# Optimization experiments

Measured on AMD Instinct MI355X. Metric: run time of the kernel, lower is better.

Reference implementation:

```python
import jax, jax.numpy as jnp
import numpy as np
import math

B, S, E, HEAD = 4, 2048, 1024, 64  # num_heads=16 -> head_size = 1024//16


def setup_inputs() -> dict:
    key = jax.random.key(0)
    kx, kp, kq, kk, kv = jax.random.split(key, 5)
    std = math.sqrt(2.0 / (E + HEAD))
    return {
        "x": jax.random.normal(kx, (B, S, E), dtype=jnp.float32),
        "padding_mask": jax.random.randint(kp, (B, S), 0, 2, dtype=jnp.int32),
        "Wq": jax.random.normal(kq, (HEAD, E), dtype=jnp.float32) * std,
        "Wk": jax.random.normal(kk, (HEAD, E), dtype=jnp.float32) * std,
        "Wv": jax.random.normal(kv, (HEAD, E), dtype=jnp.float32) * std,
    }


def reference(x, padding_mask, Wq, Wk, Wv):
    # q,k,v: [B,S,head] via Linear (x @ W.T, no bias)
    q = jnp.einsum("bse,he->bsh", x, Wq)
    k = jnp.einsum("bse,he->bsh", x, Wk)
    v = jnp.einsum("bse,he->bsh", x, Wv)
    scores = jnp.einsum("bqh,bkh->bqk", q, k)  # [B,S,S]
    seq = x.shape[1]
    causal = jnp.tril(jnp.ones((seq, seq), dtype=jnp.float32))  # [S,S]
    mask = causal[None, :, :] * padding_mask.astype(jnp.float32)[:, None, :]  # [B,S,S]
    scores = jnp.where(mask == 0, jnp.float32(-1e9), scores)
    head_size = k.shape[-1]
    attn = jax.nn.softmax(scores / jnp.sqrt(jnp.float32(head_size)), axis=-1)
    return jnp.einsum("bqk,bkh->bqh", attn, v)
```

## Files before the change

### kernel.cpp

```cpp
#include <hip/hip_runtime.h>
#include <hip/hip_bf16.h>
#include <math.h>

#define B_ 4
#define S_ 2048
#define E_ 1024
#define H_ 64
#define NQT 32
#define SPLITS 8
#define TPS 4

typedef short bf16x8 __attribute__((ext_vector_type(8)));
typedef float f32x4 __attribute__((ext_vector_type(4)));
typedef unsigned short u16x8 __attribute__((ext_vector_type(8)));
typedef unsigned short u16x4 __attribute__((ext_vector_type(4)));

__device__ __forceinline__ unsigned short f2bf(float f){
    unsigned u = __builtin_bit_cast(unsigned, f);
    u += 0x7fffu + ((u >> 16) & 1u);
    return (unsigned short)(u >> 16);
}
__device__ __forceinline__ float bf2f(unsigned short h){
    return __builtin_bit_cast(float, ((unsigned)h) << 16);
}
#define MFMA16(a,b,c) __builtin_amdgcn_mfma_f32_16x16x32_bf16((a),(b),(c),0,0,0)

__device__ __forceinline__ void gload_lds16(const void* g, void* l){
    __builtin_amdgcn_global_load_lds((const __attribute__((address_space(1))) unsigned int*)g,
                                     (__attribute__((address_space(3))) unsigned int*)l, 16, 0, 0);
}

__global__ __launch_bounds__(256) void wprep_kernel(
    const float* __restrict__ Wq, const float* __restrict__ Wk,
    const float* __restrict__ Wv,
    unsigned short* __restrict__ WhiS, unsigned short* __restrict__ WloS)
{
    const int gid = blockIdx.x*256 + threadIdx.x;
    const int n = gid >> 7, g = gid & 127;
    const float* W = (n < 64)  ? (Wq + (size_t)n*E_)
                   : (n < 128) ? (Wk + (size_t)(n-64)*E_)
                               : (Wv + (size_t)(n-128)*E_);
    const int gs = (g & ~7) | ((g & 7) ^ (n & 7));
    const float* src = W + gs*8;
    float4 a = ((const float4*)src)[0];
    float4 b = ((const float4*)src)[1];
    float vv[8] = {a.x,a.y,a.z,a.w,b.x,b.y,b.z,b.w};
    u16x8 hv, lv;
    #pragma unroll
    for (int j=0;j<8;j++){ unsigned short h = f2bf(vv[j]); hv[j]=h; lv[j]=f2bf(vv[j]-bf2f(h)); }
    ((u16x8*)WhiS)[n*128 + g] = hv;
    ((u16x8*)WloS)[n*128 + g] = lv;
}

__global__ __launch_bounds__(256) void qkv_kernel(
    const float* __restrict__ x,
    const unsigned short* __restrict__ WhiS, const unsigned short* __restrict__ WloS,
    unsigned short* __restrict__ Qhi, unsigned short* __restrict__ Qlo,
    unsigned short* __restrict__ Khi, unsigned short* __restrict__ Klo,
    unsigned short* __restrict__ Vt)
{
    __shared__ unsigned short Ah[32*64], Al[32*64];
    __shared__ unsigned short Bh[192*64], Bl[192*64];
    const int m0 = blockIdx.x * 32;
    const int tid = threadIdx.x;
    const int lane = tid & 63, wv = tid >> 6, l15 = lane & 15, quad = lane >> 4;

    f32x4 acc[2][3];
    #pragma unroll
    for (int mt=0;mt<2;mt++)
    #pragma unroll
    for (int nt=0;nt<3;nt++) acc[mt][nt] = f32x4{0.f,0.f,0.f,0.f};

    const int arow = tid >> 3;
    const int ag   = tid & 7;
    unsigned short* tbuf = (wv < 2) ? Bh : Bl;
    const unsigned short* gsrc = (wv < 2) ? WhiS : WloS;
    const int rbase0 = (wv & 1) * 96;
    const int lrow = lane >> 3, lgrp = lane & 7;

    for (int k0 = 0; k0 < E_; k0 += 64) {
        const float* xs = x + (size_t)(m0 + arow)*E_ + k0 + ag*8;
        float4 xa = ((const float4*)xs)[0];
        float4 xb = ((const float4*)xs)[1];
        __syncthreads();
        #pragma unroll
        for (int i = 0; i < 12; i++) {
            const int rb = rbase0 + i*8;
            const unsigned short* gp = gsrc + (size_t)(rb + lrow)*E_ + k0 + lgrp*8;
            gload_lds16(gp, tbuf + rb*64);
        }
        {
            float vv[8] = {xa.x,xa.y,xa.z,xa.w,xb.x,xb.y,xb.z,xb.w};
            u16x8 hv, lv;
            #pragma unroll
            for (int j=0;j<8;j++){ unsigned short h = f2bf(vv[j]); hv[j]=h; lv[j]=f2bf(vv[j]-bf2f(h)); }
            const int idx = arow*8 + (ag ^ (arow & 7));
            ((u16x8*)Ah)[idx] = hv; ((u16x8*)Al)[idx] = lv;
        }
        __syncthreads();
        #pragma unroll
        for (int kk=0; kk<2; kk++){
            const int xr = (kk*4+quad) ^ (l15 & 7);
            bf16x8 ah[2], al[2];
            #pragma unroll
            for (int mt=0; mt<2; mt++){
                const int arw = mt*16 + l15;
                ah[mt] = ((const bf16x8*)Ah)[arw*8 + xr];
                al[mt] = ((const bf16x8*)Al)[arw*8 + xr];
            }
            #pragma unroll
            for (int nt=0; nt<3; nt++){
                const int brw = wv*48 + nt*16 + l15;
                bf16x8 bh = ((const bf16x8*)Bh)[brw*8 + xr];
                bf16x8 bl = ((const bf16x8*)Bl)[brw*8 + xr];
                #pragma unroll
                for (int mt=0; mt<2; mt++){
                    acc[mt][nt] = MFMA16(ah[mt], bh, acc[mt][nt]);
                    acc[mt][nt] = MFMA16(ah[mt], bl, acc[mt][nt]);
                    acc[mt][nt] = MFMA16(al[mt], bh, acc[mt][nt]);
                }
            }
        }
    }
    #pragma unroll
    for (int nt=0; nt<3; nt++){
        const int n = wv*48 + nt*16 + l15;
        const int comp = n >> 6, c = n & 63;
        if (comp < 2) {
            unsigned short* dh = (comp==0) ? Qhi : Khi;
            unsigned short* dl = (comp==0) ? Qlo : Klo;
            #pragma unroll
            for (int mt=0; mt<2; mt++)
            #pragma unroll
            for (int r=0; r<4; r++){
                const int row = m0 + mt*16 + quad*4 + r;
                float v = acc[mt][nt][r];
                unsigned short h = f2bf(v);
                dh[(size_t)row*H_ + c] = h;
                dl[(size_t)row*H_ + c] = f2bf(v - bf2f(h));
            }
        } else {
            #pragma unroll
            for (int mt=0; mt<2; mt++){
                const int m = m0 + mt*16 + quad*4;
                const int b = m >> 11, s0 = m & (S_-1);
                u16x4 pk;
                #pragma unroll
                for (int r=0;r<4;r++) pk[r] = f2bf(acc[mt][nt][r]);
                *(u16x4*)(Vt + (size_t)(b*H_ + c)*S_ + s0) = pk;
            }
        }
    }
}

__global__ __launch_bounds__(256) void meanv_kernel(const unsigned short* __restrict__ Vt,
                                                    float* __restrict__ meanV)
{
    int b = blockIdx.x >> 6, h = blockIdx.x & 63;
    const unsigned short* src = Vt + (size_t)b*H_*S_ + (size_t)h*S_;
    float sum = 0.f;
    for (int j = threadIdx.x; j < S_; j += 256) sum += bf2f(src[j]);
    #pragma unroll
    for (int m=32; m>=1; m>>=1) sum += __shfl_xor(sum, m);
    __shared__ float red[4];
    if ((threadIdx.x & 63) == 0) red[threadIdx.x >> 6] = sum;
    __syncthreads();
    if (threadIdx.x == 0) meanV[b*H_ + h] = (red[0]+red[1]+red[2]+red[3]) * (1.f/S_);
}

__global__ __launch_bounds__(256) void attn_kernel(
    const unsigned short* __restrict__ Qhi, const unsigned short* __restrict__ Qlo,
    const unsigned short* __restrict__ Khi, const unsigned short* __restrict__ Klo,
    const unsigned short* __restrict__ Vt, const int* __restrict__ pad,
    float* __restrict__ Opart, float* __restrict__ mpart, float* __restrict__ lpart)
{
    const int qt = blockIdx.x, b = blockIdx.y, sp = blockIdx.z;
    const int t0 = sp * TPS;
    if (t0 > qt) return;
    const int t1 = min(t0 + TPS, qt + 1);

    __shared__ unsigned short Ps[4][64*20];

    const int tid = threadIdx.x, lane = tid & 63, wv = tid >> 6, l15 = lane & 15, quad = lane >> 4;

    const size_t qrow = (size_t)(b*S_ + qt*64 + wv*16 + l15);
    bf16x8 aqh0 = *(const bf16x8*)(Qhi + qrow*H_ + quad*8);
    bf16x8 aqh1 = *(const bf16x8*)(Qhi + qrow*H_ + 32 + quad*8);
    bf16x8 aql0 = *(const bf16x8*)(Qlo + qrow*H_ + quad*8);
    bf16x8 aql1 = *(const bf16x8*)(Qlo + qrow*H_ + 32 + quad*8);

    const unsigned short* KhB = Khi + (size_t)(b*S_)*H_;
    const unsigned short* KlB = Klo + (size_t)(b*S_)*H_;
    const unsigned short* VB  = Vt  + (size_t)b*H_*S_;
    const int* padB = pad + b*S_;

    float m_i[4], l_i[4];
    f32x4 o[4];
    #pragma unroll
    for (int r=0;r<4;r++){ m_i[r] = -INFINITY; l_i[r] = 0.f; }
    #pragma unroll
    for (int i=0;i<4;i++) o[i] = f32x4{0.f,0.f,0.f,0.f};

    const int qg = qt*64 + wv*16 + quad*4;
    unsigned short* Pw = &Ps[wv][0];

    for (int t = t0; t < t1; ++t) {
        const int kb = t * 64;

        int pv[4];
        #pragma unroll
        for (int nt=0; nt<4; nt++) pv[nt] = padB[kb + nt*16 + l15];

        f32x4 s[4];
        #pragma unroll
        for (int nt=0; nt<4; nt++){
            const size_t krow = (size_t)(kb + nt*16 + l15)*H_;
            bf16x8 bh0 = *(const bf16x8*)(KhB + krow + quad*8);
            bf16x8 bh1 = *(const bf16x8*)(KhB + krow + 32 + quad*8);
            bf16x8 bl0 = *(const bf16x8*)(KlB + krow + quad*8);
            bf16x8 bl1 = *(const bf16x8*)(KlB + krow + 32 + quad*8);
            f32x4 z = f32x4{0.f,0.f,0.f,0.f};
            z = MFMA16(aqh0, bh0, z);
            z = MFMA16(aqh1, bh1, z);
            z = MFMA16(aqh0, bl0, z);
            z = MFMA16(aqh1, bl1, z);
            z = MFMA16(aql0, bh0, z);
            z = MFMA16(aql1, bh1, z);
            s[nt] = z;
        }
        float rmax[4] = {-INFINITY,-INFINITY,-INFINITY,-INFINITY};
        #pragma unroll
        for (int nt=0; nt<4; nt++){
            const int kg = kb + nt*16 + l15;
            #pragma unroll
            for (int r=0;r<4;r++){
                bool ok = (kg <= qg + r) && (pv[nt] != 0);
                float v = ok ? s[nt][r]*0.125f : -1.25e8f;
                s[nt][r] = v;
                rmax[r] = fmaxf(rmax[r], v);
            }
        }
        #pragma unroll
        for (int msk=1; msk<=8; msk<<=1){
            #pragma unroll
            for (int r=0;r<4;r++) rmax[r] = fmaxf(rmax[r], __shfl_xor(rmax[r], msk));
        }
        float alpha[4];
        #pragma unroll
        for (int r=0;r<4;r++){
            float mn = fmaxf(m_i[r], rmax[r]);
            alpha[r] = __expf(m_i[r] - mn);
            m_i[r] = mn;
        }
        float rsum[4] = {0.f,0.f,0.f,0.f};
        #pragma unroll
        for (int nt=0; nt<4; nt++)
        #pragma unroll
        for (int r=0;r<4;r++){
            float p = __expf(s[nt][r] - m_i[r]);
            s[nt][r] = p;
            rsum[r] += p;
        }
        #pragma unroll
        for (int msk=1; msk<=8; msk<<=1){
            #pragma unroll
            for (int r=0;r<4;r++) rsum[r] += __shfl_xor(rsum[r], msk);
        }
        #pragma unroll
        for (int r=0;r<4;r++) l_i[r] = l_i[r]*alpha[r] + rsum[r];
        #pragma unroll
        for (int hnt=0; hnt<4; hnt++)
        #pragma unroll
        for (int r=0;r<4;r++) o[hnt][r] *= alpha[r];

        #pragma unroll
        for (int nt=0; nt<4; nt++){
            const int key = nt*16 + l15;
            u16x4 pk;
            #pragma unroll
            for (int r=0;r<4;r++) pk[r] = f2bf(s[nt][r]);
            *(u16x4*)(Pw + key*20 + quad*4) = pk;
        }
        #pragma unroll
        for (int ks=0; ks<2; ks++){
            bf16x8 ap;
            #pragma unroll
            for (int j=0;j<8;j++) ap[j] = (short)Pw[(ks*32 + quad*8 + j)*20 + l15];
            #pragma unroll
            for (int hnt=0; hnt<4; hnt++){
                bf16x8 bv = *(const bf16x8*)(VB + (size_t)(hnt*16 + l15)*S_ + kb + ks*32 + quad*8);
                o[hnt] = MFMA16(ap, bv, o[hnt]);
            }
        }
    }
    const size_t rbase = ((size_t)((b*NQT + qt)*SPLITS + sp))*64 + wv*16 + quad*4;
    if (l15 == 0) {
        #pragma unroll
        for (int r=0;r<4;r++){ mpart[rbase + r] = m_i[r]; lpart[rbase + r] = l_i[r]; }
    }
    #pragma unroll
    for (int hnt=0; hnt<4; hnt++)
    #pragma unroll
    for (int r=0;r<4;r++)
        Opart[(rbase + r)*H_ + hnt*16 + l15] = o[hnt][r];
}

__global__ __launch_bounds__(256) void combine_kernel(
    const float* __restrict__ Opart, const float* __restrict__ mpart,
    const float* __restrict__ lpart, const float* __restrict__ meanV,
    float* __restrict__ out)
{
    const int idx = blockIdx.x*256 + threadIdx.x;
    const int h = idx & 63;
    const int q = (idx >> 6) & (S_-1);
    const int b = idx >> 17;
    const int qt = q >> 6, r = q & 63;
    const int ns = (qt >> 2) + 1;
    const size_t rb = ((size_t)(b*NQT + qt)*SPLITS)*64 + r;
    float M = -INFINITY;
    for (int s2=0; s2<ns; s2++) M = fmaxf(M, mpart[rb + (size_t)s2*64]);
    float res;
    if (M == -1.25e8f) {
        res = meanV[b*H_ + h];
    } else {
        float L = 0.f, acc = 0.f;
        for (int s2=0; s2<ns; s2++){
            float mi = mpart[rb + (size_t)s2*64];
            float wgt = __expf(mi - M);
            L += wgt * lpart[rb + (size_t)s2*64];
            acc += wgt * Opart[(rb + (size_t)s2*64)*H_ + h];
        }
        res = acc / L;
    }
    out[idx] = res;
}

extern "C" void kernel_launch(void* const* d_in, const int* in_sizes, int n_in,
                              void* d_out, int out_size, void* d_ws, size_t ws_size,
                              hipStream_t stream)
{
    (void)in_sizes; (void)n_in; (void)out_size; (void)ws_size;
    const float* x  = (const float*)d_in[0];
    const int* pad  = (const int*)d_in[1];
    const float* Wq = (const float*)d_in[2];
    const float* Wk = (const float*)d_in[3];
    const float* Wv = (const float*)d_in[4];
    float* out = (float*)d_out;
    char* ws = (char*)d_ws;
    const size_t MB = 1u << 20;
    unsigned short* Qhi = (unsigned short*)(ws + 0*MB);
    unsigned short* Qlo = (unsigned short*)(ws + 1*MB);
    unsigned short* Khi = (unsigned short*)(ws + 2*MB);
    unsigned short* Klo = (unsigned short*)(ws + 3*MB);
    unsigned short* Vt  = (unsigned short*)(ws + 4*MB);
    float* Opart = (float*)(ws + 5*MB);
    float* mpart = (float*)(ws + 21*MB);
    float* lpart = (float*)(ws + 21*MB + (1u<<18));
    float* meanV = (float*)(ws + 21*MB + 2*(1u<<18));
    unsigned short* WhiS = (unsigned short*)(ws + 22*MB);
    unsigned short* WloS = (unsigned short*)(ws + 22*MB + 512*1024);

    wprep_kernel<<<dim3(96), 256, 0, stream>>>(Wq, Wk, Wv, WhiS, WloS);
    qkv_kernel<<<dim3(256), 256, 0, stream>>>(x, WhiS, WloS, Qhi, Qlo, Khi, Klo, Vt);
    meanv_kernel<<<dim3(256), 256, 0, stream>>>(Vt, meanV);
    attn_kernel<<<dim3(NQT, B_, SPLITS), 256, 0, stream>>>(Qhi, Qlo, Khi, Klo, Vt, pad,
                                                           Opart, mpart, lpart);
    combine_kernel<<<dim3((B_*S_*H_)/256), 256, 0, stream>>>(Opart, mpart, lpart, meanV, out);
}
```

Before: 162.2 us.

## Stage K/V tiles through double-buffered swizzled LDS with register prefetch

Each block now loads its K-hi, K-lo, V and padding tiles cooperatively into double-buffered shared memory. Three wavefronts each fetch one tensor and the fourth fetches the mask, and the next tile is prefetched into registers during compute. The previous code had every wavefront read all four K/V tiles straight from global memory, so the same data was fetched four times per block. The XOR swizzle is meant to avoid LDS bank conflicts, and the causal comparison is skipped on off-diagonal tiles. In exchange it uses about 50KB of LDS, which may lower occupancy, and adds a block barrier per tile.

Measured after the change: 142.3 us. 12.3% less time.

```diff
diff --git a/kernel.cpp b/kernel.cpp
--- a/kernel.cpp
+++ b/kernel.cpp
@@ -179,9 +179,12 @@
     if (t0 > qt) return;
     const int t1 = min(t0 + TPS, qt + 1);
 
+    __shared__ unsigned short KtH[2][64*64], KtL[2][64*64], Vts[2][64*64];
     __shared__ unsigned short Ps[4][64*20];
+    __shared__ int pad_s[2][64];
 
     const int tid = threadIdx.x, lane = tid & 63, wv = tid >> 6, l15 = lane & 15, quad = lane >> 4;
+    const int role = tid >> 6, srow = tid & 63;
 
     const size_t qrow = (size_t)(b*S_ + qt*64 + wv*16 + l15);
     bf16x8 aqh0 = *(const bf16x8*)(Qhi + qrow*H_ + quad*8);
@@ -204,21 +207,52 @@
     const int qg = qt*64 + wv*16 + quad*4;
     unsigned short* Pw = &Ps[wv][0];
 
+    u16x8 stg[8];
+    int pvreg = 0;
+    auto issue = [&](int t){
+        const int kb = t * 64;
+        if (role < 3) {
+            const unsigned short* gs =
+                (role==0) ? (KhB + (size_t)(kb + srow)*H_) :
+                (role==1) ? (KlB + (size_t)(kb + srow)*H_) :
+                            (VB + (size_t)srow*S_ + kb);
+            #pragma unroll
+            for (int i=0;i<8;i++) stg[i] = ((const u16x8*)gs)[i];
+        } else {
+            pvreg = padB[kb + srow];
+        }
+    };
+    auto commit = [&](int buf){
+        if (role < 3) {
+            unsigned short* ld = (role==0) ? &KtH[buf][0] : (role==1) ? &KtL[buf][0] : &Vts[buf][0];
+            #pragma unroll
+            for (int i=0;i<8;i++) ((u16x8*)ld)[srow*8 + (i ^ (srow & 7))] = stg[i];
+        } else {
+            pad_s[buf][srow] = pvreg;
+        }
+    };
+
+    issue(t0); commit(0);
+    __syncthreads();
+    int cur = 0;
+
     for (int t = t0; t < t1; ++t) {
         const int kb = t * 64;
+        const bool hasnext = (t + 1 < t1);
+        if (hasnext) issue(t + 1);
 
         int pv[4];
         #pragma unroll
-        for (int nt=0; nt<4; nt++) pv[nt] = padB[kb + nt*16 + l15];
+        for (int nt=0; nt<4; nt++) pv[nt] = pad_s[cur][nt*16 + l15];
 
         f32x4 s[4];
         #pragma unroll
         for (int nt=0; nt<4; nt++){
-            const size_t krow = (size_t)(kb + nt*16 + l15)*H_;
-            bf16x8 bh0 = *(const bf16x8*)(KhB + krow + quad*8);
-            bf16x8 bh1 = *(const bf16x8*)(KhB + krow + 32 + quad*8);
-            bf16x8 bl0 = *(const bf16x8*)(KlB + krow + quad*8);
-            bf16x8 bl1 = *(const bf16x8*)(KlB + krow + 32 + quad*8);
+            const int krw = nt*16 + l15;
+            bf16x8 bh0 = ((const bf16x8*)&KtH[cur][0])[krw*8 + ((quad)   ^ (l15 & 7))];
+            bf16x8 bh1 = ((const bf16x8*)&KtH[cur][0])[krw*8 + ((4+quad) ^ (l15 & 7))];
+            bf16x8 bl0 = ((const bf16x8*)&KtL[cur][0])[krw*8 + ((quad)   ^ (l15 & 7))];
+            bf16x8 bl1 = ((const bf16x8*)&KtL[cur][0])[krw*8 + ((4+quad) ^ (l15 & 7))];
             f32x4 z = f32x4{0.f,0.f,0.f,0.f};
             z = MFMA16(aqh0, bh0, z);
             z = MFMA16(aqh1, bh1, z);
@@ -229,15 +263,28 @@
             s[nt] = z;
         }
         float rmax[4] = {-INFINITY,-INFINITY,-INFINITY,-INFINITY};
-        #pragma unroll
-        for (int nt=0; nt<4; nt++){
-            const int kg = kb + nt*16 + l15;
-            #pragma unroll
-            for (int r=0;r<4;r++){
-                bool ok = (kg <= qg + r) && (pv[nt] != 0);
-                float v = ok ? s[nt][r]*0.125f : -1.25e8f;
-                s[nt][r] = v;
-                rmax[r] = fmaxf(rmax[r], v);
+        if (t == qt) {
+            #pragma unroll
+            for (int nt=0; nt<4; nt++){
+                const int kg = kb + nt*16 + l15;
+                #pragma unroll
+                for (int r=0;r<4;r++){
+                    bool ok = (kg <= qg + r) && (pv[nt] != 0);
+                    float v = ok ? s[nt][r]*0.125f : -1.25e8f;
+                    s[nt][r] = v;
+                    rmax[r] = fmaxf(rmax[r], v);
+                }
+            }
+        } else {
+            #pragma unroll
+            for (int nt=0; nt<4; nt++){
+                const bool ok = (pv[nt] != 0);
+                #pragma unroll
+                for (int r=0;r<4;r++){
+                    float v = ok ? s[nt][r]*0.125f : -1.25e8f;
+                    s[nt][r] = v;
+                    rmax[r] = fmaxf(rmax[r], v);
+                }
             }
         }
         #pragma unroll
@@ -288,9 +335,15 @@
             for (int j=0;j<8;j++) ap[j] = (short)Pw[(ks*32 + quad*8 + j)*20 + l15];
             #pragma unroll
             for (int hnt=0; hnt<4; hnt++){
-                bf16x8 bv = *(const bf16x8*)(VB + (size_t)(hnt*16 + l15)*S_ + kb + ks*32 + quad*8);
+                bf16x8 bv = ((const bf16x8*)&Vts[cur][0])[(hnt*16+l15)*8 + ((ks*4+quad) ^ (l15 & 7))];
                 o[hnt] = MFMA16(ap, bv, o[hnt]);
             }
+        }
+
+        if (hasnext) {
+            commit(cur ^ 1);
+            __syncthreads();
+            cur ^= 1;
         }
     }
     const size_t rbase = ((size_t)((b*NQT + qt)*SPLITS + sp))*64 + wv*16 + quad*4;
```
